# Kernel tuning notes

Measured on AMD Instinct MI355X. Metric: run time of the kernel, lower is better.

The kernel has to match this reference:

```python
import jax, jax.numpy as jnp
import numpy as np

N_NODES = 4_194_304
N_GRAPHS = 65_536

# Orthonormal (Frobenius) basis for symmetric traceless 3x3 matrices: the
# real l=2 components of 1o x 1o -> 2e (Clebsch-Gordan up to basis choice).
_s2 = 1.0 / np.sqrt(2.0)
_B = np.zeros((5, 3, 3), dtype=np.float32)
_B[0, 0, 1] = _B[0, 1, 0] = _s2            # xy
_B[1, 1, 2] = _B[1, 2, 1] = _s2            # yz
_B[2, 0, 2] = _B[2, 2, 0] = _s2            # xz
_B[3, 0, 0] = _s2; _B[3, 1, 1] = -_s2      # x^2 - y^2
_B[4, 0, 0] = _B[4, 1, 1] = -1.0 / np.sqrt(6.0); _B[4, 2, 2] = 2.0 / np.sqrt(6.0)
B_CG = jnp.asarray(_B)

INV_SQRT2 = 0.7071067811865476
INV_SQRT3 = 0.5773502691896258


def setup_inputs() -> dict:
    key = jax.random.key(0)
    k1, k2, k3, k4, k5, k6 = jax.random.split(key, 6)
    z = jax.random.randint(k1, (N_NODES,), 0, 100, dtype=jnp.int32)
    pos = jax.random.normal(k2, (N_NODES, 3), dtype=jnp.float32)
    batch = jnp.sort(jax.random.randint(k3, (N_NODES,), 0, N_GRAPHS, dtype=jnp.int32))
    # FullyConnectedTensorProduct weights: 5 paths, mul pattern (1,1,mul_out)
    # 0e*0e->2x0e (2) + 1o*1o->2x0e (2) + 0e*1o->2x1o (2) + 1o*0e->2x1o (2) + 1o*1o->1x2e (1) = 9
    w_tp = jax.random.normal(k4, (9,), dtype=jnp.float32)
    fc_w = jax.random.normal(k5, (1, 13), dtype=jnp.float32) / np.sqrt(13.0)
    fc_b = jax.random.normal(k6, (1,), dtype=jnp.float32) * 0.01
    return {"z": z, "pos": pos, "batch": batch, "w_tp": w_tp, "fc_w": fc_w, "fc_b": fc_b}


def reference(z, pos, batch, w_tp, fc_w, fc_b):
    s = z.astype(jnp.float32)                      # [N] scalar (0e) part
    v = pos                                        # [N,3] vector (1o) part
    wA, wB = w_tp[0:2], w_tp[2:4]                  # -> 2x0e paths
    wC, wD = w_tp[4:6], w_tp[6:8]                  # -> 2x1o paths
    wE = w_tp[8]                                   # -> 1x2e path

    # CG tensor product x (x) x -> 2x0e + 2x1o + 1x2e, path-normalized by 1/sqrt(#paths)
    ss = s * s                                     # 0e x 0e -> 0e
    dot = jnp.sum(v * v, axis=-1)                  # 1o . 1o -> 0e (CG = delta/sqrt3)
    out0 = (ss[:, None] * wA + (dot * INV_SQRT3)[:, None] * wB) * INV_SQRT2   # [N,2]
    sv = s[:, None] * v                            # 0e x 1o -> 1o
    out1 = (sv[:, None, :] * (wC + wD)[None, :, None]) * INV_SQRT2            # [N,2,3]
    quad = jnp.einsum('kij,ni,nj->nk', B_CG, v, v) # 1o x 1o -> 2e            # [N,5]
    out2 = wE * quad

    x = jnp.concatenate([out0, out1.reshape(-1, 6), out2], axis=-1)  # [N,13]
    x = jax.nn.relu(x)                             # (as in source: relu on all irreps)
    y = x @ fc_w.T + fc_b                          # [N,1] -> 1x0e
    y = jnp.tanh(y)                                # Gate on pure scalars = scalar act

    sums = jax.ops.segment_sum(y, batch, num_segments=N_GRAPHS)                # [G,1]
    counts = jax.ops.segment_sum(jnp.ones((batch.shape[0], 1), y.dtype), batch,
                                 num_segments=N_GRAPHS)
    return sums / jnp.maximum(counts, 1.0)
```

## Files before the change

kernel.cpp:

```cpp
#include <hip/hip_runtime.h>

static constexpr float INV_SQRT2 = 0.70710678118654752f;
static constexpr float INV_SQRT3 = 0.57735026918962576f;
static constexpr float SQRT2     = 1.41421356237309505f;
static constexpr float INV_SQRT6 = 0.40824829046386302f;

static constexpr int W_GRAPHS = 8;
static constexpr int B_GRAPHS = 32;

__device__ __forceinline__ float fast_tanh(float x) {
    const float e = __builtin_amdgcn_exp2f(x * 2.8853900817779268f);
    const float r = __builtin_amdgcn_rcpf(e + 1.0f);
    return fmaf(-2.0f, r, 1.0f);
}

__device__ __forceinline__ float gate_p(float k, float fw) { return k > 0.f ? k * fw : 0.f; }
__device__ __forceinline__ float gate_n(float k, float fw) { return k < 0.f ? k * fw : 0.f; }

__global__ __launch_bounds__(256) void e3nn_fused(
    const int*   __restrict__ z,
    const float* __restrict__ pos,
    const int*   __restrict__ batch,
    const float* __restrict__ w_tp,
    const float* __restrict__ fc_w,
    const float* __restrict__ fc_b,
    float*       __restrict__ out,
    int n, int n_graphs)
{
    const int tid  = threadIdx.x;
    const int wid  = tid >> 6;
    const int lane = tid & 63;
    const int bg0  = blockIdx.x * B_GRAPHS;
    if (bg0 >= n_graphs) return;

    __shared__ int sbnd[B_GRAPHS + 1];

    if (wid == 0) {
        const int tl     = (lane < B_GRAPHS) ? lane : B_GRAPHS;
        const int target = bg0 + tl;
        unsigned p2 = 1;
        while (p2 < (unsigned)n) p2 <<= 1;
        int bv = 0;
        for (unsigned step = p2 >> 1; step > 0; step >>= 1) {
            const unsigned cand = (unsigned)bv + step;
            if (cand <= (unsigned)n && batch[cand - 1] < target) bv = (int)cand;
        }
        if (lane <= B_GRAPHS) sbnd[lane] = bv;
    }
    __syncthreads();

    const float kA0 = w_tp[0] * INV_SQRT2;
    const float kA1 = w_tp[1] * INV_SQRT2;
    const float kB0 = w_tp[2] * (INV_SQRT3 * INV_SQRT2);
    const float kB1 = w_tp[3] * (INV_SQRT3 * INV_SQRT2);
    const float c0  = (w_tp[4] + w_tp[6]) * INV_SQRT2;
    const float c1  = (w_tp[5] + w_tp[7]) * INV_SQRT2;
    const float wE  = w_tp[8];
    const float fw0 = fc_w[0], fw1 = fc_w[1];
    const float fb  = fc_b[0];

    const float P0 = gate_p(c0, fc_w[2]) + gate_p(c1, fc_w[5]);
    const float N0 = gate_n(c0, fc_w[2]) + gate_n(c1, fc_w[5]);
    const float P1 = gate_p(c0, fc_w[3]) + gate_p(c1, fc_w[6]);
    const float N1 = gate_n(c0, fc_w[3]) + gate_n(c1, fc_w[6]);
    const float P2 = gate_p(c0, fc_w[4]) + gate_p(c1, fc_w[7]);
    const float N2 = gate_n(c0, fc_w[4]) + gate_n(c1, fc_w[7]);
    const float k8  = wE * SQRT2,     k11 = wE * INV_SQRT2, k12 = wE * INV_SQRT6;
    const float P8  = gate_p(k8,  fc_w[8]),  N8  = gate_n(k8,  fc_w[8]);
    const float P9  = gate_p(k8,  fc_w[9]),  N9  = gate_n(k8,  fc_w[9]);
    const float P10 = gate_p(k8,  fc_w[10]), N10 = gate_n(k8,  fc_w[10]);
    const float P11 = gate_p(k11, fc_w[11]), N11 = gate_n(k11, fc_w[11]);
    const float P12 = gate_p(k12, fc_w[12]), N12 = gate_n(k12, fc_w[12]);

    const int wb   = wid * W_GRAPHS;
    const int B0 = sbnd[wb + 0], B1 = sbnd[wb + 1];
    const int B2 = sbnd[wb + 2], B3 = sbnd[wb + 3];
    const int B4 = sbnd[wb + 4], B5 = sbnd[wb + 5];
    const int B6 = sbnd[wb + 6], B7 = sbnd[wb + 7];
    const int B8 = sbnd[wb + 8];
    const int myb = sbnd[wb + ((lane < W_GRAPHS) ? lane : W_GRAPHS)];
    const int nbv = sbnd[wb + ((lane < W_GRAPHS) ? lane + 1 : W_GRAPHS)];

    float a0 = 0.f, a1 = 0.f, a2 = 0.f, a3 = 0.f;
    float a4 = 0.f, a5 = 0.f, a6 = 0.f, a7 = 0.f;

#pragma unroll 1
    for (int base = B0; base < B8; base += 64) {
        const int i = base + lane;
        if (i < B8) {
            const float sc = (float)z[i];
            const float v0 = pos[i * 3 + 0];
            const float v1 = pos[i * 3 + 1];
            const float v2 = pos[i * 3 + 2];

            const float v00 = v0 * v0, v11 = v1 * v1, v22 = v2 * v2;
            const float ss  = sc * sc;
            const float dr  = v00 + v11 + v22;

            float acc = fb;
            const float x0 = fmaf(ss, kA0, dr * kB0);
            const float x1 = fmaf(ss, kA1, dr * kB1);
            acc = fmaf(fmaxf(x0, 0.f), fw0, acc);
            acc = fmaf(fmaxf(x1, 0.f), fw1, acc);

            const float sv0 = sc * v0, sv1 = sc * v1, sv2 = sc * v2;
            acc = fmaf(sv0, (sv0 > 0.f ? P0 : N0), acc);
            acc = fmaf(sv1, (sv1 > 0.f ? P1 : N1), acc);
            acc = fmaf(sv2, (sv2 > 0.f ? P2 : N2), acc);

            const float t8 = v0 * v1, t9 = v1 * v2, t10 = v0 * v2;
            acc = fmaf(t8,  (t8  > 0.f ? P8  : N8 ), acc);
            acc = fmaf(t9,  (t9  > 0.f ? P9  : N9 ), acc);
            acc = fmaf(t10, (t10 > 0.f ? P10 : N10), acc);

            const float t11 = v00 - v11;
            acc = fmaf(t11, (t11 > 0.f ? P11 : N11), acc);
            const float t12 = (v22 - v00) + (v22 - v11);
            acc = fmaf(t12, (t12 > 0.f ? P12 : N12), acc);

            const float y = fast_tanh(acc);

            const bool ge1 = i >= B1, ge2 = i >= B2, ge3 = i >= B3;
            const bool ge4 = i >= B4, ge5 = i >= B5, ge6 = i >= B6;
            const bool ge7 = i >= B7;
            a0 += (!ge1)        ? y : 0.f;
            a1 += (ge1 && !ge2) ? y : 0.f;
            a2 += (ge2 && !ge3) ? y : 0.f;
            a3 += (ge3 && !ge4) ? y : 0.f;
            a4 += (ge4 && !ge5) ? y : 0.f;
            a5 += (ge5 && !ge6) ? y : 0.f;
            a6 += (ge6 && !ge7) ? y : 0.f;
            a7 += (ge7)         ? y : 0.f;
        }
    }

#pragma unroll
    for (int off = 32; off >= 1; off >>= 1) {
        a0 += __shfl_xor(a0, off);
        a1 += __shfl_xor(a1, off);
        a2 += __shfl_xor(a2, off);
        a3 += __shfl_xor(a3, off);
        a4 += __shfl_xor(a4, off);
        a5 += __shfl_xor(a5, off);
        a6 += __shfl_xor(a6, off);
        a7 += __shfl_xor(a7, off);
    }

    const int gw0 = bg0 + wid * W_GRAPHS;
    if (lane < W_GRAPHS && gw0 + lane < n_graphs) {
        float sel = (lane == 0) ? a0
                  : (lane == 1) ? a1
                  : (lane == 2) ? a2
                  : (lane == 3) ? a3
                  : (lane == 4) ? a4
                  : (lane == 5) ? a5
                  : (lane == 6) ? a6
                  :               a7;
        const float c = (float)(nbv - myb);
        out[gw0 + lane] = sel / fmaxf(c, 1.0f);
    }
}

extern "C" void kernel_launch(void* const* d_in, const int* in_sizes, int n_in,
                              void* d_out, int out_size, void* d_ws, size_t ws_size,
                              hipStream_t stream) {
    const int*   z     = (const int*)d_in[0];
    const float* pos   = (const float*)d_in[1];
    const int*   batch = (const int*)d_in[2];
    const float* w_tp  = (const float*)d_in[3];
    const float* fc_w  = (const float*)d_in[4];
    const float* fc_b  = (const float*)d_in[5];

    float* out = (float*)d_out;
    const int n        = in_sizes[0];
    const int n_graphs = out_size;

    const int blocks = (n_graphs + B_GRAPHS - 1) / B_GRAPHS;
    e3nn_fused<<<blocks, 256, 0, stream>>>(z, pos, batch, w_tp, fc_w, fc_b,
                                           out, n, n_graphs);
}
```

Before: 26.31 us.

## Prefetch node data into LDS with async global_load_lds double-buffering

```diff
diff --git a/kernel.cpp b/kernel.cpp
--- a/kernel.cpp
+++ b/kernel.cpp
@@ -7,6 +7,7 @@
 
 static constexpr int W_GRAPHS = 8;
 static constexpr int B_GRAPHS = 32;
+static constexpr int NSLOT    = 4;
 
 __device__ __forceinline__ float fast_tanh(float x) {
     const float e = __builtin_amdgcn_exp2f(x * 2.8853900817779268f);
@@ -16,6 +17,9 @@
 
 __device__ __forceinline__ float gate_p(float k, float fw) { return k > 0.f ? k * fw : 0.f; }
 __device__ __forceinline__ float gate_n(float k, float fw) { return k < 0.f ? k * fw : 0.f; }
+
+typedef const __attribute__((address_space(1))) void gvoid_t;
+typedef __attribute__((address_space(3))) void lvoid_t;
 
 __global__ __launch_bounds__(256) void e3nn_fused(
     const int*   __restrict__ z,
@@ -33,7 +37,9 @@
     const int bg0  = blockIdx.x * B_GRAPHS;
     if (bg0 >= n_graphs) return;
 
-    __shared__ int sbnd[B_GRAPHS + 1];
+    __shared__ int   sbnd[B_GRAPHS + 1];
+    __shared__ int   zb[4][NSLOT][64];
+    __shared__ float pb[4][NSLOT][3][64];
 
     if (wid == 0) {
         const int tl     = (lane < B_GRAPHS) ? lane : B_GRAPHS;
@@ -72,7 +78,7 @@
     const float P11 = gate_p(k11, fc_w[11]), N11 = gate_n(k11, fc_w[11]);
     const float P12 = gate_p(k12, fc_w[12]), N12 = gate_n(k12, fc_w[12]);
 
-    const int wb   = wid * W_GRAPHS;
+    const int wb = wid * W_GRAPHS;
     const int B0 = sbnd[wb + 0], B1 = sbnd[wb + 1];
     const int B2 = sbnd[wb + 2], B3 = sbnd[wb + 3];
     const int B4 = sbnd[wb + 4], B5 = sbnd[wb + 5];
@@ -81,70 +87,107 @@
     const int myb = sbnd[wb + ((lane < W_GRAPHS) ? lane : W_GRAPHS)];
     const int nbv = sbnd[wb + ((lane < W_GRAPHS) ? lane + 1 : W_GRAPHS)];
 
-    float a0 = 0.f, a1 = 0.f, a2 = 0.f, a3 = 0.f;
-    float a4 = 0.f, a5 = 0.f, a6 = 0.f, a7 = 0.f;
+    const int T = (B8 - B0) >> 6;
+
+    auto stage = [&](int s) {
+        const int sl = s & (NSLOT - 1);
+        const int gi = B0 + (s << 6) + lane;
+        __builtin_amdgcn_global_load_lds((gvoid_t*)(z + gi),
+                                         (lvoid_t*)&zb[wid][sl][0], 4, 0, 0);
+        __builtin_amdgcn_global_load_lds((gvoid_t*)(pos + 3 * gi + 0),
+                                         (lvoid_t*)&pb[wid][sl][0][0], 4, 0, 0);
+        __builtin_amdgcn_global_load_lds((gvoid_t*)(pos + 3 * gi + 1),
+                                         (lvoid_t*)&pb[wid][sl][1][0], 4, 0, 0);
+        __builtin_amdgcn_global_load_lds((gvoid_t*)(pos + 3 * gi + 2),
+                                         (lvoid_t*)&pb[wid][sl][2][0], 4, 0, 0);
+    };
+
+    if (T > 0) stage(0);
+    if (T > 1) stage(1);
+
+    float tot = 0.f, s1 = 0.f, s2 = 0.f, s3 = 0.f;
+    float s4  = 0.f, s5 = 0.f, s6 = 0.f, s7 = 0.f;
+
+    auto body = [&](int i, float sc, float v0, float v1, float v2, bool valid) {
+        const float v00 = v0 * v0, v11 = v1 * v1, v22 = v2 * v2;
+        const float ss  = sc * sc;
+        const float dr  = v00 + v11 + v22;
+
+        float acc = fb;
+        const float x0 = fmaf(ss, kA0, dr * kB0);
+        const float x1 = fmaf(ss, kA1, dr * kB1);
+        acc = fmaf(fmaxf(x0, 0.f), fw0, acc);
+        acc = fmaf(fmaxf(x1, 0.f), fw1, acc);
+
+        const float sv0 = sc * v0, sv1 = sc * v1, sv2 = sc * v2;
+        acc = fmaf(sv0, (sv0 > 0.f ? P0 : N0), acc);
+        acc = fmaf(sv1, (sv1 > 0.f ? P1 : N1), acc);
+        acc = fmaf(sv2, (sv2 > 0.f ? P2 : N2), acc);
+
+        const float t8 = v0 * v1, t9 = v1 * v2, t10 = v0 * v2;
+        acc = fmaf(t8,  (t8  > 0.f ? P8  : N8 ), acc);
+        acc = fmaf(t9,  (t9  > 0.f ? P9  : N9 ), acc);
+        acc = fmaf(t10, (t10 > 0.f ? P10 : N10), acc);
+
+        const float t11 = v00 - v11;
+        acc = fmaf(t11, (t11 > 0.f ? P11 : N11), acc);
+        const float t12 = (v22 - v00) + (v22 - v11);
+        acc = fmaf(t12, (t12 > 0.f ? P12 : N12), acc);
+
+        float y = fast_tanh(acc);
+        if (!valid) y = 0.f;
+
+        tot += y;
+        s1 += (i >= B1) ? y : 0.f;
+        s2 += (i >= B2) ? y : 0.f;
+        s3 += (i >= B3) ? y : 0.f;
+        s4 += (i >= B4) ? y : 0.f;
+        s5 += (i >= B5) ? y : 0.f;
+        s6 += (i >= B6) ? y : 0.f;
+        s7 += (i >= B7) ? y : 0.f;
+    };
 
 #pragma unroll 1
-    for (int base = B0; base < B8; base += 64) {
-        const int i = base + lane;
-        if (i < B8) {
-            const float sc = (float)z[i];
-            const float v0 = pos[i * 3 + 0];
-            const float v1 = pos[i * 3 + 1];
-            const float v2 = pos[i * 3 + 2];
-
-            const float v00 = v0 * v0, v11 = v1 * v1, v22 = v2 * v2;
-            const float ss  = sc * sc;
-            const float dr  = v00 + v11 + v22;
-
-            float acc = fb;
-            const float x0 = fmaf(ss, kA0, dr * kB0);
-            const float x1 = fmaf(ss, kA1, dr * kB1);
-            acc = fmaf(fmaxf(x0, 0.f), fw0, acc);
-            acc = fmaf(fmaxf(x1, 0.f), fw1, acc);
-
-            const float sv0 = sc * v0, sv1 = sc * v1, sv2 = sc * v2;
-            acc = fmaf(sv0, (sv0 > 0.f ? P0 : N0), acc);
-            acc = fmaf(sv1, (sv1 > 0.f ? P1 : N1), acc);
-            acc = fmaf(sv2, (sv2 > 0.f ? P2 : N2), acc);
-
-            const float t8 = v0 * v1, t9 = v1 * v2, t10 = v0 * v2;
-            acc = fmaf(t8,  (t8  > 0.f ? P8  : N8 ), acc);
-            acc = fmaf(t9,  (t9  > 0.f ? P9  : N9 ), acc);
-            acc = fmaf(t10, (t10 > 0.f ? P10 : N10), acc);
-
-            const float t11 = v00 - v11;
-            acc = fmaf(t11, (t11 > 0.f ? P11 : N11), acc);
-            const float t12 = (v22 - v00) + (v22 - v11);
-            acc = fmaf(t12, (t12 > 0.f ? P12 : N12), acc);
-
-            const float y = fast_tanh(acc);
-
-            const bool ge1 = i >= B1, ge2 = i >= B2, ge3 = i >= B3;
-            const bool ge4 = i >= B4, ge5 = i >= B5, ge6 = i >= B6;
-            const bool ge7 = i >= B7;
-            a0 += (!ge1)        ? y : 0.f;
-            a1 += (ge1 && !ge2) ? y : 0.f;
-            a2 += (ge2 && !ge3) ? y : 0.f;
-            a3 += (ge3 && !ge4) ? y : 0.f;
-            a4 += (ge4 && !ge5) ? y : 0.f;
-            a5 += (ge5 && !ge6) ? y : 0.f;
-            a6 += (ge6 && !ge7) ? y : 0.f;
-            a7 += (ge7)         ? y : 0.f;
+    for (int t = 0; t < T; ++t) {
+        if (t + 1 < T) { asm volatile("s_waitcnt vmcnt(4)" ::: "memory"); }
+        else           { asm volatile("s_waitcnt vmcnt(0)" ::: "memory"); }
+        __builtin_amdgcn_sched_barrier(0);
+        const int sl = t & (NSLOT - 1);
+        const float sc = (float)zb[wid][sl][lane];
+        const float v0 = pb[wid][sl][0][lane];
+        const float v1 = pb[wid][sl][1][lane];
+        const float v2 = pb[wid][sl][2][lane];
+        if (t + 2 < T) stage(t + 2);
+        body(B0 + (t << 6) + lane, sc, v0, v1, v2, true);
+    }
+
+    {
+        const int tb = B0 + (T << 6);
+        if (tb < B8) {
+            const int i = tb + lane;
+            float sc = 0.f, v0 = 0.f, v1 = 0.f, v2 = 0.f;
+            if (i < B8) {
+                sc = (float)z[i];
+                v0 = pos[3 * i]; v1 = pos[3 * i + 1]; v2 = pos[3 * i + 2];
+            }
+            body(i, sc, v0, v1, v2, i < B8);
         }
     }
 
 #pragma unroll
     for (int off = 32; off >= 1; off >>= 1) {
-        a0 += __shfl_xor(a0, off);
-        a1 += __shfl_xor(a1, off);
-        a2 += __shfl_xor(a2, off);
-        a3 += __shfl_xor(a3, off);
-        a4 += __shfl_xor(a4, off);
-        a5 += __shfl_xor(a5, off);
-        a6 += __shfl_xor(a6, off);
-        a7 += __shfl_xor(a7, off);
-    }
+        tot += __shfl_xor(tot, off);
+        s1  += __shfl_xor(s1,  off);
+        s2  += __shfl_xor(s2,  off);
+        s3  += __shfl_xor(s3,  off);
+        s4  += __shfl_xor(s4,  off);
+        s5  += __shfl_xor(s5,  off);
+        s6  += __shfl_xor(s6,  off);
+        s7  += __shfl_xor(s7,  off);
+    }
+
+    const float a0 = tot - s1, a1 = s1 - s2, a2 = s2 - s3, a3 = s3 - s4;
+    const float a4 = s4 - s5,  a5 = s5 - s6, a6 = s6 - s7, a7 = s7;
 
     const int gw0 = bg0 + wid * W_GRAPHS;
     if (lane < W_GRAPHS && gw0 + lane < n_graphs) {
```

Measured after the change: 27.88 us. 1.06x slower.
